# Optimization experiments

Hardware: AMD Instinct MI355X
Metric: run time of the kernel (lower is better)

The kernel has to match this reference:

```python
import jax, jax.numpy as jnp
import numpy as np

SIZE = 128   # feature dim
N = 4096     # number of mesh nodes


def setup_inputs() -> dict:
    key = jax.random.key(0)
    k_f, k_adj, k_q, k_k = jax.random.split(key, 4)
    # f: [size, N] node features (features-first, as in the torch module); scaled
    # so QK dot products stay O(1) and exp() is numerically safe.
    f = jax.random.normal(k_f, (SIZE, N), dtype=jnp.float32) * 0.1
    # neighbors: [N, N] binary adjacency with self-loops (every row sums > 0).
    adj = (jax.random.uniform(k_adj, (N, N)) < 0.005).astype(jnp.float32)
    neighbors = jnp.maximum(adj, jnp.eye(N, dtype=jnp.float32))
    # learned per-feature scale vectors (nn.init.normal_)
    wq = jax.random.normal(k_q, (SIZE,), dtype=jnp.float32)
    wk = jax.random.normal(k_k, (SIZE,), dtype=jnp.float32)
    return {"f": f, "neighbors": neighbors, "wq": wq, "wk": wk}


def reference(f, neighbors, wq, wk):
    # elementwise-scaled queries/keys: [size, N]
    wq_f = wq[:, None] * f
    wk_f = wk[:, None] * f
    # S[i, j] = exp(<wq_f[:, i], wk_f[:, j]>)  -> [N, N]
    S = jnp.exp(jnp.einsum('dn,dm->nm', wq_f, wk_f))
    # normalize by neighbor-sums: S / (neighbors @ S).T
    S = S / jnp.matmul(neighbors, S).T
    return S
```

## Files before the change

kernel.cpp:

```cpp
#include <hip/hip_runtime.h>
#include <hip/hip_fp16.h>

#define N    4096
#define SIZE 128
#define CAP  128
#define RB   16
#define TB   1024

typedef __attribute__((ext_vector_type(8))) _Float16 f16x8;
typedef __attribute__((ext_vector_type(2))) __fp16 fp16x2;
typedef __attribute__((ext_vector_type(4))) float f32x4;

__device__ __forceinline__ unsigned int pk2(float lo, float hi) {
    union { fp16x2 v; unsigned int u; } c;
    c.v = __builtin_amdgcn_cvt_pkrtz(lo, hi);
    return c.u;
}
__device__ __forceinline__ __half2 u2h(unsigned int u) {
    union { unsigned int u; __half2 h; } c; c.u = u; return c.h;
}

__global__ __launch_bounds__(256)
void setup(const float* __restrict__ nb, const float* __restrict__ f,
           const float* __restrict__ wq, const float* __restrict__ wk,
           int* __restrict__ cnt8, int* __restrict__ idx,
           _Float16* __restrict__ Af, _Float16* __restrict__ Bf) {
    __shared__ int   wtot[4];
    __shared__ float sf[SIZE][16];
    __shared__ float sqw[SIZE];
    const int t = threadIdx.x;

    if (blockIdx.x < N) {
        const int j    = blockIdx.x;
        const int lane = t & 63;
        const int wv   = t >> 6;
        const float4* row4 = (const float4*)(nb + (size_t)j * N);
        int* irow = idx + (size_t)j * CAP;

        float4 v[4];
#pragma unroll
        for (int it = 0; it < 4; ++it) v[it] = row4[t + it * 256];

        unsigned int msk = 0u;
#pragma unroll
        for (int it = 0; it < 4; ++it) {
            const float e[4] = {v[it].x, v[it].y, v[it].z, v[it].w};
#pragma unroll
            for (int q = 0; q < 4; ++q)
                if (e[q] != 0.0f) msk |= 1u << (it * 4 + q);
        }
        const int cnt = __popc(msk);
        int scan = cnt;
#pragma unroll
        for (int s = 1; s < 64; s <<= 1) {
            const int o = __shfl_up(scan, s);
            if (lane >= s) scan += o;
        }
        if (lane == 63) wtot[wv] = scan;
        __syncthreads();
        int base = 0;
#pragma unroll
        for (int w = 0; w < 3; ++w)
            if (w < wv) base += wtot[w];
        int p = base + scan - cnt;
        unsigned int m = msk;
        while (m) {
            const int b = __ffs(m) - 1;
            m &= m - 1u;
            const int c = 4 * (t + (b >> 2) * 256) + (b & 3);
            if (p < CAP) irow[p] = c;
            ++p;
        }
        if (t == 255) {
            int n = base + scan;
            if (n > CAP) n = CAP;
            const int n8 = (n + 7) & ~7;
            for (int q = n; q < n8; ++q) irow[q] = N;
            cnt8[j] = n8 >> 3;
        }
    } else {
        const int tile = blockIdx.x - N;
        if (t < SIZE) sqw[t] = wq[t] * wk[t];
        const int col0 = t & 15;
#pragma unroll
        for (int it = 0; it < 8; ++it) {
            const int k = (t >> 4) + it * 16;
            sf[k][col0] = f[(size_t)k * N + tile * 16 + col0];
        }
        __syncthreads();
        const int ks   = t >> 6;
        const int lane = t & 63;
        const int quad = lane >> 4;
        const int col  = lane & 15;
        f16x8 va, vb;
#pragma unroll
        for (int jj = 0; jj < 8; ++jj) {
            const int k = ks * 32 + quad * 8 + jj;
            const float v = sf[k][col];
            va[jj] = (_Float16)(sqw[k] * v);
            vb[jj] = (_Float16)v;
        }
        const size_t o = (size_t)(tile * 4 + ks) * 64 + lane;
        ((f16x8*)Af)[o] = va;
        ((f16x8*)Bf)[o] = vb;
    }
}

__global__ __launch_bounds__(TB, 4)
void fused(const _Float16* __restrict__ Af, const _Float16* __restrict__ Bf,
           const int* __restrict__ cnt8, const int* __restrict__ idx,
           float* __restrict__ out) {
    __shared__ uint4 Sb[2 * N + 3];
    uint4* const sA = Sb;
    uint4* const sB = Sb + N + 2;
    const int t    = threadIdx.x;
    const int lane = t & 63;
    const int wv   = t >> 6;
    const int quad = lane >> 4;
    const int i0   = blockIdx.x * RB;

    if (t == 0) {
        sA[N] = make_uint4(0u, 0u, 0u, 0u);
        sB[N] = make_uint4(0u, 0u, 0u, 0u);
    }

    int cc = cnt8[t];
    const int4* ir0 = (const int4*)(idx + (size_t)t * CAP);
    int4 ka = ir0[0];
    int4 kb = ir0[1];

    f16x8 af[4];
    const f16x8* Ap = (const f16x8*)Af + (size_t)blockIdx.x * 4 * 64;
#pragma unroll
    for (int ks = 0; ks < 4; ++ks) af[ks] = Ap[ks * 64 + lane];
    const f16x8* Bp = (const f16x8*)Bf;

#pragma unroll 4
    for (int ti = 0; ti < 16; ++ti) {
        const int nt = wv * 16 + ti;
        f32x4 acc = {0.f, 0.f, 0.f, 0.f};
#pragma unroll
        for (int ks = 0; ks < 4; ++ks) {
            const f16x8 bfrag = Bp[(size_t)(nt * 4 + ks) * 64 + lane];
            acc = __builtin_amdgcn_mfma_f32_16x16x32_f16(af[ks], bfrag, acc, 0, 0, 0);
        }
        const int j = nt * 16 + (lane & 15);
        uint2 pp;
        pp.x = pk2(__expf(acc[0]), __expf(acc[1]));
        pp.y = pk2(__expf(acc[2]), __expf(acc[3]));
        uint2* bs = (quad < 2) ? (uint2*)&sA[j] : (uint2*)&sB[j];
        bs[quad & 1] = pp;
    }
    __syncthreads();

#define ACC(D, A, B) \
    D[0] = __hadd2(D[0], u2h((A).x)); D[1] = __hadd2(D[1], u2h((A).y)); \
    D[2] = __hadd2(D[2], u2h((A).z)); D[3] = __hadd2(D[3], u2h((A).w)); \
    D[4] = __hadd2(D[4], u2h((B).x)); D[5] = __hadd2(D[5], u2h((B).y)); \
    D[6] = __hadd2(D[6], u2h((B).z)); D[7] = __hadd2(D[7], u2h((B).w));

    for (int u = 0; u < 4; ++u) {
        const int j = t + u * TB;
        const int4* ir = (const int4*)(idx + (size_t)j * CAP);
        int ncc = 0; int4 nk0 = ka, nk1 = kb;
        if (u < 3) {
            const int jn = j + TB;
            const int4* irn = (const int4*)(idx + (size_t)jn * CAP);
            ncc = cnt8[jn];
            nk0 = irn[0];
            nk1 = irn[1];
        }
        __half2 d0[8], d1[8], d2[8], d3[8];
        const __half2 z = u2h(0u);
#pragma unroll
        for (int r = 0; r < 8; ++r) { d0[r] = z; d1[r] = z; d2[r] = z; d3[r] = z; }

        for (int c = 0; c < cc; ++c) {
            int4 pa = ka, pb = kb;
            if (c + 1 < cc) { pa = ir[2 * c + 2]; pb = ir[2 * c + 3]; }
            const uint4 ax = sA[ka.x], bx = sB[ka.x];
            const uint4 ay = sA[ka.y], by = sB[ka.y];
            const uint4 az = sA[ka.z], bz = sB[ka.z];
            const uint4 aw = sA[ka.w], bw = sB[ka.w];
            const uint4 ex = sA[kb.x], fx = sB[kb.x];
            const uint4 ey = sA[kb.y], fy = sB[kb.y];
            const uint4 ez = sA[kb.z], fz = sB[kb.z];
            const uint4 ew = sA[kb.w], fw = sB[kb.w];
            ACC(d0, ax, bx)
            ACC(d1, ay, by)
            ACC(d0, az, bz)
            ACC(d1, aw, bw)
            ACC(d2, ex, fx)
            ACC(d3, ey, fy)
            ACC(d2, ez, fz)
            ACC(d3, ew, fw)
            ka = pa; kb = pb;
        }
        const uint4 na4 = sA[j], nb4 = sB[j];
        const unsigned int nu[8] = {na4.x, na4.y, na4.z, na4.w,
                                    nb4.x, nb4.y, nb4.z, nb4.w};
#pragma unroll
        for (int i = 0; i < 8; ++i) {
            const __half2 dd = __hadd2(__hadd2(d0[i], d1[i]), __hadd2(d2[i], d3[i]));
            const __half2 nn = u2h(nu[i]);
            out[(size_t)(i0 + 2 * i + 0) * N + j] =
                __low2float(nn)  * __builtin_amdgcn_rcpf(__low2float(dd));
            out[(size_t)(i0 + 2 * i + 1) * N + j] =
                __high2float(nn) * __builtin_amdgcn_rcpf(__high2float(dd));
        }
        cc = ncc; ka = nk0; kb = nk1;
    }
#undef ACC
}

extern "C" void kernel_launch(void* const* d_in, const int* in_sizes, int n_in,
                              void* d_out, int out_size, void* d_ws, size_t ws_size,
                              hipStream_t stream) {
    const float* f  = (const float*)d_in[0];
    const float* nb = (const float*)d_in[1];
    const float* wq = (const float*)d_in[2];
    const float* wk = (const float*)d_in[3];
    float* out = (float*)d_out;

    int*      cnt8 = (int*)d_ws;
    int*      idx  = cnt8 + N;
    _Float16* Af   = (_Float16*)(idx + (size_t)N * CAP);
    _Float16* Bf   = Af + (size_t)256 * 4 * 64 * 8;

    setup<<<N + 256, 256, 0, stream>>>(nb, f, wq, wk, cnt8, idx, Af, Bf);
    fused<<<N / RB, TB, 0, stream>>>(Af, Bf, cnt8, idx, out);
}
```

Before: 145.8 us.

## Halve rows per block, drop self-loop from index list, use nontemporal stores

Each block now handles 8 query rows instead of 16, which halves the shared-memory S tile and the half2 accumulators so more blocks can be resident (launch bounds raised to 8 waves per SIMD). The diagonal self-loop is removed from the neighbor lists and added back from the already-loaded own value, and the lists get an extra padding group so the prefetch no longer needs a bounds branch. Output stores become nontemporal. In exchange, the grid doubles and every block recomputes the full QK^T tile while keeping only half of it, so MFMA and exp work per output roughly doubles.

```diff
diff --git a/kernel.cpp b/kernel.cpp
--- a/kernel.cpp
+++ b/kernel.cpp
@@ -1,11 +1,12 @@
 #include <hip/hip_runtime.h>
 #include <hip/hip_fp16.h>
 
-#define N    4096
-#define SIZE 128
-#define CAP  128
-#define RB   16
-#define TB   1024
+#define N     4096
+#define SIZE  128
+#define CAP   128
+#define NMAX  120
+#define RB    8
+#define TB    1024
 
 typedef __attribute__((ext_vector_type(8))) _Float16 f16x8;
 typedef __attribute__((ext_vector_type(2))) __fp16 fp16x2;
@@ -23,7 +24,7 @@
 __global__ __launch_bounds__(256)
 void setup(const float* __restrict__ nb, const float* __restrict__ f,
            const float* __restrict__ wq, const float* __restrict__ wk,
-           int* __restrict__ cnt8, int* __restrict__ idx,
+           int* __restrict__ cnt, int* __restrict__ idx,
            _Float16* __restrict__ Af, _Float16* __restrict__ Bf) {
     __shared__ int   wtot[4];
     __shared__ float sf[SIZE][16];
@@ -49,8 +50,10 @@
             for (int q = 0; q < 4; ++q)
                 if (e[q] != 0.0f) msk |= 1u << (it * 4 + q);
         }
-        const int cnt = __popc(msk);
-        int scan = cnt;
+        if (((j >> 2) & 255) == t) msk &= ~(1u << ((j >> 10) * 4 + (j & 3)));
+
+        const int pc = __popc(msk);
+        int scan = pc;
 #pragma unroll
         for (int s = 1; s < 64; s <<= 1) {
             const int o = __shfl_up(scan, s);
@@ -62,21 +65,21 @@
 #pragma unroll
         for (int w = 0; w < 3; ++w)
             if (w < wv) base += wtot[w];
-        int p = base + scan - cnt;
+        int p = base + scan - pc;
         unsigned int m = msk;
         while (m) {
             const int b = __ffs(m) - 1;
             m &= m - 1u;
             const int c = 4 * (t + (b >> 2) * 256) + (b & 3);
-            if (p < CAP) irow[p] = c;
+            if (p < NMAX) irow[p] = c;
             ++p;
         }
         if (t == 255) {
             int n = base + scan;
-            if (n > CAP) n = CAP;
+            if (n > NMAX) n = NMAX;
             const int n8 = (n + 7) & ~7;
-            for (int q = n; q < n8; ++q) irow[q] = N;
-            cnt8[j] = n8 >> 3;
+            for (int q = n; q < n8 + 8; ++q) irow[q] = N;
+            cnt[j] = n8 >> 3;
         }
     } else {
         const int tile = blockIdx.x - N;
@@ -106,34 +109,31 @@
     }
 }
 
-__global__ __launch_bounds__(TB, 4)
+__global__ __launch_bounds__(TB, 8)
 void fused(const _Float16* __restrict__ Af, const _Float16* __restrict__ Bf,
-           const int* __restrict__ cnt8, const int* __restrict__ idx,
+           const int* __restrict__ cnt, const int* __restrict__ idx,
            float* __restrict__ out) {
-    __shared__ uint4 Sb[2 * N + 3];
-    uint4* const sA = Sb;
-    uint4* const sB = Sb + N + 2;
+    __shared__ uint4 sA[N + 2];
     const int t    = threadIdx.x;
     const int lane = t & 63;
     const int wv   = t >> 6;
     const int quad = lane >> 4;
-    const int i0   = blockIdx.x * RB;
-
-    if (t == 0) {
-        sA[N] = make_uint4(0u, 0u, 0u, 0u);
-        sB[N] = make_uint4(0u, 0u, 0u, 0u);
-    }
-
-    int cc = cnt8[t];
+    const int bid  = blockIdx.x;
+    const int i0   = bid * RB;
+
+    if (t == 0) sA[N] = make_uint4(0u, 0u, 0u, 0u);
+
+    int cc = cnt[t];
     const int4* ir0 = (const int4*)(idx + (size_t)t * CAP);
     int4 ka = ir0[0];
     int4 kb = ir0[1];
 
     f16x8 af[4];
-    const f16x8* Ap = (const f16x8*)Af + (size_t)blockIdx.x * 4 * 64;
+    const f16x8* Ap = (const f16x8*)Af + (size_t)(bid >> 1) * 4 * 64;
 #pragma unroll
     for (int ks = 0; ks < 4; ++ks) af[ks] = Ap[ks * 64 + lane];
     const f16x8* Bp = (const f16x8*)Bf;
+    const bool sel = (quad >> 1) == (bid & 1);
 
 #pragma unroll 4
     for (int ti = 0; ti < 16; ++ti) {
@@ -144,20 +144,19 @@
             const f16x8 bfrag = Bp[(size_t)(nt * 4 + ks) * 64 + lane];
             acc = __builtin_amdgcn_mfma_f32_16x16x32_f16(af[ks], bfrag, acc, 0, 0, 0);
         }
-        const int j = nt * 16 + (lane & 15);
-        uint2 pp;
-        pp.x = pk2(__expf(acc[0]), __expf(acc[1]));
-        pp.y = pk2(__expf(acc[2]), __expf(acc[3]));
-        uint2* bs = (quad < 2) ? (uint2*)&sA[j] : (uint2*)&sB[j];
-        bs[quad & 1] = pp;
+        if (sel) {
+            const int j = nt * 16 + (lane & 15);
+            uint2 pp;
+            pp.x = pk2(__expf(acc[0]), __expf(acc[1]));
+            pp.y = pk2(__expf(acc[2]), __expf(acc[3]));
+            ((uint2*)&sA[j])[quad & 1] = pp;
+        }
     }
     __syncthreads();
 
-#define ACC(D, A, B) \
+#define ACC4(D, A) \
     D[0] = __hadd2(D[0], u2h((A).x)); D[1] = __hadd2(D[1], u2h((A).y)); \
-    D[2] = __hadd2(D[2], u2h((A).z)); D[3] = __hadd2(D[3], u2h((A).w)); \
-    D[4] = __hadd2(D[4], u2h((B).x)); D[5] = __hadd2(D[5], u2h((B).y)); \
-    D[6] = __hadd2(D[6], u2h((B).z)); D[7] = __hadd2(D[7], u2h((B).w));
+    D[2] = __hadd2(D[2], u2h((A).z)); D[3] = __hadd2(D[3], u2h((A).w));
 
     for (int u = 0; u < 4; ++u) {
         const int j = t + u * TB;
@@ -166,51 +165,43 @@
         if (u < 3) {
             const int jn = j + TB;
             const int4* irn = (const int4*)(idx + (size_t)jn * CAP);
-            ncc = cnt8[jn];
+            ncc = cnt[jn];
             nk0 = irn[0];
             nk1 = irn[1];
         }
-        __half2 d0[8], d1[8], d2[8], d3[8];
+        __half2 d0[4], d1[4], d2[4], d3[4];
         const __half2 z = u2h(0u);
 #pragma unroll
-        for (int r = 0; r < 8; ++r) { d0[r] = z; d1[r] = z; d2[r] = z; d3[r] = z; }
+        for (int r = 0; r < 4; ++r) { d0[r] = z; d1[r] = z; d2[r] = z; d3[r] = z; }
 
         for (int c = 0; c < cc; ++c) {
-            int4 pa = ka, pb = kb;
-            if (c + 1 < cc) { pa = ir[2 * c + 2]; pb = ir[2 * c + 3]; }
-            const uint4 ax = sA[ka.x], bx = sB[ka.x];
-            const uint4 ay = sA[ka.y], by = sB[ka.y];
-            const uint4 az = sA[ka.z], bz = sB[ka.z];
-            const uint4 aw = sA[ka.w], bw = sB[ka.w];
-            const uint4 ex = sA[kb.x], fx = sB[kb.x];
-            const uint4 ey = sA[kb.y], fy = sB[kb.y];
-            const uint4 ez = sA[kb.z], fz = sB[kb.z];
-            const uint4 ew = sA[kb.w], fw = sB[kb.w];
-            ACC(d0, ax, bx)
-            ACC(d1, ay, by)
-            ACC(d0, az, bz)
-            ACC(d1, aw, bw)
-            ACC(d2, ex, fx)
-            ACC(d3, ey, fy)
-            ACC(d2, ez, fz)
-            ACC(d3, ew, fw)
+            const int4 pa = ir[2 * c + 2];
+            const int4 pb = ir[2 * c + 3];
+            const uint4 ax = sA[ka.x], ay = sA[ka.y];
+            const uint4 az = sA[ka.z], aw = sA[ka.w];
+            const uint4 ex = sA[kb.x], ey = sA[kb.y];
+            const uint4 ez = sA[kb.z], ew = sA[kb.w];
+            ACC4(d0, ax) ACC4(d1, ay) ACC4(d0, az) ACC4(d1, aw)
+            ACC4(d2, ex) ACC4(d3, ey) ACC4(d2, ez) ACC4(d3, ew)
             ka = pa; kb = pb;
         }
-        const uint4 na4 = sA[j], nb4 = sB[j];
-        const unsigned int nu[8] = {na4.x, na4.y, na4.z, na4.w,
-                                    nb4.x, nb4.y, nb4.z, nb4.w};
-#pragma unroll
-        for (int i = 0; i < 8; ++i) {
-            const __half2 dd = __hadd2(__hadd2(d0[i], d1[i]), __hadd2(d2[i], d3[i]));
+        const uint4 nn4 = sA[j];
+        const unsigned int nu[4] = {nn4.x, nn4.y, nn4.z, nn4.w};
+#pragma unroll
+        for (int i = 0; i < 4; ++i) {
             const __half2 nn = u2h(nu[i]);
-            out[(size_t)(i0 + 2 * i + 0) * N + j] =
-                __low2float(nn)  * __builtin_amdgcn_rcpf(__low2float(dd));
-            out[(size_t)(i0 + 2 * i + 1) * N + j] =
-                __high2float(nn) * __builtin_amdgcn_rcpf(__high2float(dd));
+            __half2 dd = __hadd2(__hadd2(d0[i], d1[i]), __hadd2(d2[i], d3[i]));
+            dd = __hadd2(dd, nn);
+            __builtin_nontemporal_store(
+                __low2float(nn)  * __builtin_amdgcn_rcpf(__low2float(dd)),
+                &out[(size_t)(i0 + 2 * i + 0) * N + j]);
+            __builtin_nontemporal_store(
+                __high2float(nn) * __builtin_amdgcn_rcpf(__high2float(dd)),
+                &out[(size_t)(i0 + 2 * i + 1) * N + j]);
         }
         cc = ncc; ka = nk0; kb = nk1;
     }
-#undef ACC
+#undef ACC4
 }
 
 extern "C" void kernel_launch(void* const* d_in, const int* in_sizes, int n_in,
@@ -222,11 +213,11 @@
     const float* wk = (const float*)d_in[3];
     float* out = (float*)d_out;
 
-    int*      cnt8 = (int*)d_ws;
-    int*      idx  = cnt8 + N;
-    _Float16* Af   = (_Float16*)(idx + (size_t)N * CAP);
-    _Float16* Bf   = Af + (size_t)256 * 4 * 64 * 8;
-
-    setup<<<N + 256, 256, 0, stream>>>(nb, f, wq, wk, cnt8, idx, Af, Bf);
-    fused<<<N / RB, TB, 0, stream>>>(Af, Bf, cnt8, idx, out);
-}
+    int*      cnt = (int*)d_ws;
+    int*      idx = cnt + N;
+    _Float16* Af  = (_Float16*)(idx + (size_t)N * CAP);
+    _Float16* Bf  = Af + (size_t)256 * 4 * 64 * 8;
+
+    setup<<<N + 256, 256, 0, stream>>>(nb, f, wq, wk, cnt, idx, Af, Bf);
+    fused<<<N / RB, TB, 0, stream>>>(Af, Bf, cnt, idx, out);
+}
```

Result: slower. 199.7 us (+37.0%).

## Compact adjacency one row per wavefront and handle self-loop implicitly

Applied to the files above, without the earlier changes.

The setup kernel now gives each adjacency row to a single wavefront (four rows per block) and drops the cross-wave shared-memory scan and barrier. The diagonal entry is removed from the neighbor list and added back directly in the normalization. This can cut one 8-wide gather group for rows whose count lands on a multiple of eight. The gather loop now prefetches unconditionally, with extra padding past the end of each list, so the per-iteration branch goes away. The extra padding and the cap of 120 neighbors keep the prefetch in bounds, but rows with more neighbors would be truncated.

```diff
diff --git a/kernel.cpp b/kernel.cpp
--- a/kernel.cpp
+++ b/kernel.cpp
@@ -1,11 +1,12 @@
 #include <hip/hip_runtime.h>
 #include <hip/hip_fp16.h>
 
-#define N    4096
-#define SIZE 128
-#define CAP  128
-#define RB   16
-#define TB   1024
+#define N     4096
+#define SIZE  128
+#define CAP   128
+#define NMAX  120
+#define RB    16
+#define TB    1024
 
 typedef __attribute__((ext_vector_type(8))) _Float16 f16x8;
 typedef __attribute__((ext_vector_type(2))) __fp16 fp16x2;
@@ -23,63 +24,58 @@
 __global__ __launch_bounds__(256)
 void setup(const float* __restrict__ nb, const float* __restrict__ f,
            const float* __restrict__ wq, const float* __restrict__ wk,
-           int* __restrict__ cnt8, int* __restrict__ idx,
+           int* __restrict__ cnt, int* __restrict__ idx,
            _Float16* __restrict__ Af, _Float16* __restrict__ Bf) {
-    __shared__ int   wtot[4];
     __shared__ float sf[SIZE][16];
     __shared__ float sqw[SIZE];
     const int t = threadIdx.x;
 
-    if (blockIdx.x < N) {
-        const int j    = blockIdx.x;
+    if (blockIdx.x < N / 4) {
         const int lane = t & 63;
         const int wv   = t >> 6;
+        const int j    = blockIdx.x * 4 + wv;
         const float4* row4 = (const float4*)(nb + (size_t)j * N);
         int* irow = idx + (size_t)j * CAP;
 
-        float4 v[4];
-#pragma unroll
-        for (int it = 0; it < 4; ++it) v[it] = row4[t + it * 256];
-
-        unsigned int msk = 0u;
-#pragma unroll
-        for (int it = 0; it < 4; ++it) {
-            const float e[4] = {v[it].x, v[it].y, v[it].z, v[it].w};
+        float4 v[16];
+#pragma unroll
+        for (int s = 0; s < 16; ++s) v[s] = row4[s * 64 + lane];
+
+        unsigned long long m = 0ull;
+#pragma unroll
+        for (int s = 0; s < 16; ++s) {
+            const float e[4] = {v[s].x, v[s].y, v[s].z, v[s].w};
 #pragma unroll
             for (int q = 0; q < 4; ++q)
-                if (e[q] != 0.0f) msk |= 1u << (it * 4 + q);
-        }
-        const int cnt = __popc(msk);
-        int scan = cnt;
+                if (e[q] != 0.0f) m |= 1ull << (s * 4 + q);
+        }
+        if (((j >> 2) & 63) == lane) m &= ~(1ull << ((j >> 8) * 4 + (j & 3)));
+
+        const int pc = __popcll(m);
+        int scan = pc;
 #pragma unroll
         for (int s = 1; s < 64; s <<= 1) {
             const int o = __shfl_up(scan, s);
             if (lane >= s) scan += o;
         }
-        if (lane == 63) wtot[wv] = scan;
-        __syncthreads();
-        int base = 0;
-#pragma unroll
-        for (int w = 0; w < 3; ++w)
-            if (w < wv) base += wtot[w];
-        int p = base + scan - cnt;
-        unsigned int m = msk;
-        while (m) {
-            const int b = __ffs(m) - 1;
-            m &= m - 1u;
-            const int c = 4 * (t + (b >> 2) * 256) + (b & 3);
-            if (p < CAP) irow[p] = c;
+        int p = scan - pc;
+        unsigned long long mm = m;
+        while (mm) {
+            const int b = __ffsll(mm) - 1;
+            mm &= mm - 1ull;
+            const int c = 4 * ((b >> 2) * 64 + lane) + (b & 3);
+            if (p < NMAX) irow[p] = c;
             ++p;
         }
-        if (t == 255) {
-            int n = base + scan;
-            if (n > CAP) n = CAP;
+        if (lane == 63) {
+            int n = scan;
+            if (n > NMAX) n = NMAX;
             const int n8 = (n + 7) & ~7;
-            for (int q = n; q < n8; ++q) irow[q] = N;
-            cnt8[j] = n8 >> 3;
+            for (int q = n; q < n8 + 8; ++q) irow[q] = N;
+            cnt[j] = n8 >> 3;
         }
     } else {
-        const int tile = blockIdx.x - N;
+        const int tile = blockIdx.x - N / 4;
         if (t < SIZE) sqw[t] = wq[t] * wk[t];
         const int col0 = t & 15;
 #pragma unroll
@@ -108,7 +104,7 @@
 
 __global__ __launch_bounds__(TB, 4)
 void fused(const _Float16* __restrict__ Af, const _Float16* __restrict__ Bf,
-           const int* __restrict__ cnt8, const int* __restrict__ idx,
+           const int* __restrict__ cnt, const int* __restrict__ idx,
            float* __restrict__ out) {
     __shared__ uint4 Sb[2 * N + 3];
     uint4* const sA = Sb;
@@ -124,7 +120,7 @@
         sB[N] = make_uint4(0u, 0u, 0u, 0u);
     }
 
-    int cc = cnt8[t];
+    int cc = cnt[t];
     const int4* ir0 = (const int4*)(idx + (size_t)t * CAP);
     int4 ka = ir0[0];
     int4 kb = ir0[1];
@@ -166,7 +162,7 @@
         if (u < 3) {
             const int jn = j + TB;
             const int4* irn = (const int4*)(idx + (size_t)jn * CAP);
-            ncc = cnt8[jn];
+            ncc = cnt[jn];
             nk0 = irn[0];
             nk1 = irn[1];
         }
@@ -176,8 +172,8 @@
         for (int r = 0; r < 8; ++r) { d0[r] = z; d1[r] = z; d2[r] = z; d3[r] = z; }
 
         for (int c = 0; c < cc; ++c) {
-            int4 pa = ka, pb = kb;
-            if (c + 1 < cc) { pa = ir[2 * c + 2]; pb = ir[2 * c + 3]; }
+            const int4 pa = ir[2 * c + 2];
+            const int4 pb = ir[2 * c + 3];
             const uint4 ax = sA[ka.x], bx = sB[ka.x];
             const uint4 ay = sA[ka.y], by = sB[ka.y];
             const uint4 az = sA[ka.z], bz = sB[ka.z];
@@ -201,8 +197,9 @@
                                     nb4.x, nb4.y, nb4.z, nb4.w};
 #pragma unroll
         for (int i = 0; i < 8; ++i) {
-            const __half2 dd = __hadd2(__hadd2(d0[i], d1[i]), __hadd2(d2[i], d3[i]));
             const __half2 nn = u2h(nu[i]);
+            __half2 dd = __hadd2(__hadd2(d0[i], d1[i]), __hadd2(d2[i], d3[i]));
+            dd = __hadd2(dd, nn);
             out[(size_t)(i0 + 2 * i + 0) * N + j] =
                 __low2float(nn)  * __builtin_amdgcn_rcpf(__low2float(dd));
             out[(size_t)(i0 + 2 * i + 1) * N + j] =
@@ -222,11 +219,11 @@
     const float* wk = (const float*)d_in[3];
     float* out = (float*)d_out;
 
-    int*      cnt8 = (int*)d_ws;
-    int*      idx  = cnt8 + N;
-    _Float16* Af   = (_Float16*)(idx + (size_t)N * CAP);
-    _Float16* Bf   = Af + (size_t)256 * 4 * 64 * 8;
-
-    setup<<<N + 256, 256, 0, stream>>>(nb, f, wq, wk, cnt8, idx, Af, Bf);
-    fused<<<N / RB, TB, 0, stream>>>(Af, Bf, cnt8, idx, out);
-}
+    int*      cnt = (int*)d_ws;
+    int*      idx = cnt + N;
+    _Float16* Af  = (_Float16*)(idx + (size_t)N * CAP);
+    _Float16* Bf  = Af + (size_t)256 * 4 * 64 * 8;
+
+    setup<<<N / 4 + 256, 256, 0, stream>>>(nb, f, wq, wk, cnt, idx, Af, Bf);
+    fused<<<N / RB, TB, 0, stream>>>(Af, Bf, cnt, idx, out);
+}
```

Measured after the change: 147.8 us. About the same (+1.4%).
